# Kernel optimization log

Hardware: AMD Instinct MI355X
Metric: run time of the kernel (lower is better)

The kernel has to match this reference:

```python
import jax, jax.numpy as jnp
import numpy as np

CUT_DIST = 4.0            # cut_dist_bohr
FEATURES = 20
EPSILON = 1e-11
BOHR = 0.5291772105638411  # distance_mul (ase.units.Bohr)
POS_SCALE = 2.5


def setup_inputs() -> dict:
    key = jax.random.key(0)
    k1, k2 = jax.random.split(key)
    source = jax.random.normal(k1, (1, 4096, 3), dtype=jnp.float32) * POS_SCALE
    target = jax.random.normal(k2, (1, 2048, 3), dtype=jnp.float32) * POS_SCALE
    return {"source": source, "target": target}


def reference(source, target):
    # Pairwise diff between every source (probe) and target (atom): [B, N, M, 3]
    diff = target[:, None, :, :] - source[:, :, None, :]
    dist = jnp.sqrt(jnp.sum(diff * diff, axis=-1))            # [B, N, M]
    mask = dist < CUT_DIST                                    # [B, N, M] bool (self_send=True keeps d==0)
    direction = diff / (dist[..., None] + EPSILON)            # [B, N, M, 3]
    # sinc radial basis expansion on distances converted with distance_mul (Bohr)
    d = dist * BOHR + EPSILON                                 # [B, N, M]
    n = jnp.arange(1, FEATURES + 1, dtype=d.dtype)            # [F]
    d_exp = d[..., None]                                      # [B, N, M, 1]
    expansion = jnp.sin(n * jnp.pi * d_exp / CUT_DIST) / d_exp  # [B, N, M, F]
    return dist, direction, mask, expansion
```

## Files before the change

kernel.cpp:

```cpp
#include <hip/hip_runtime.h>
#include <math.h>

#define TILE 256
#define NFEAT 20

__global__ __launch_bounds__(256) void deepdft_expansion_kernel(
    const float* __restrict__ src,
    const float* __restrict__ tgt,
    float* __restrict__ out,
    unsigned int N, unsigned int M)
{
    const float CUT  = 4.0f;
    const float EPS  = 1e-11f;
    const float BOHR = 0.5291772105638411f;
    const float PI_F = 3.14159265358979323846f;

    const unsigned int total = N * M;

    float* __restrict__ dist_o = out;
    float* __restrict__ dir_o  = out + (size_t)total;
    float* __restrict__ mask_o = out + (size_t)4 * total;
    float* __restrict__ exp_o  = out + (size_t)5 * total;

    __shared__ float lds_dir[TILE * 3];
    __shared__ float lds_x[TILE];
    __shared__ float lds_invd[TILE];

    const unsigned int tid = threadIdx.x;
    const unsigned int tiles = (total + TILE - 1) / TILE;

    for (unsigned int tile = blockIdx.x; tile < tiles; tile += gridDim.x) {
        const unsigned int base = tile * TILE;
        const unsigned int idx  = base + tid;

        if (idx < total) {
            unsigned int n = idx / M;
            unsigned int m = idx - n * M;

            float sx = src[3u*n + 0], sy = src[3u*n + 1], sz = src[3u*n + 2];
            float tx = tgt[3u*m + 0], ty = tgt[3u*m + 1], tz = tgt[3u*m + 2];

            float dx = tx - sx, dy = ty - sy, dz = tz - sz;
            float d2   = fmaf(dx, dx, fmaf(dy, dy, dz * dz));
            float dist = sqrtf(d2);
            float inv  = 1.0f / (dist + EPS);

            dist_o[idx] = dist;
            mask_o[idx] = (dist < CUT) ? 1.0f : 0.0f;

            lds_dir[3u*tid + 0] = dx * inv;
            lds_dir[3u*tid + 1] = dy * inv;
            lds_dir[3u*tid + 2] = dz * inv;

            float d = fmaf(dist, BOHR, EPS);
            lds_invd[tid] = 1.0f / d;
            lds_x[tid]    = (PI_F / CUT) * d;
        }
        __syncthreads();

        {
            float* gdir = dir_o + (size_t)3 * base;
            #pragma unroll
            for (int k = 0; k < 3; ++k) {
                unsigned int e = tid + (unsigned)k * TILE;
                unsigned int p = (e * 10923u) >> 15;
                if (base + p < total) gdir[e] = lds_dir[e];
            }
        }

        {
            float4* gexp = reinterpret_cast<float4*>(exp_o + (size_t)NFEAT * base);
            #pragma unroll
            for (int k = 0; k < 5; ++k) {
                unsigned int j = tid + (unsigned)k * TILE;
                unsigned int p = (j * 6554u) >> 15;
                unsigned int g = j - 5u * p;
                if (base + p < total) {
                    float x    = lds_x[p];
                    float invd = lds_invd[p];
                    float n0   = (float)(4u * g + 1u);
                    float4 v;
                    v.x = __sinf( n0          * x) * invd;
                    v.y = __sinf((n0 + 1.0f)  * x) * invd;
                    v.z = __sinf((n0 + 2.0f)  * x) * invd;
                    v.w = __sinf((n0 + 3.0f)  * x) * invd;
                    gexp[j] = v;
                }
            }
        }
        __syncthreads();
    }
}

extern "C" void kernel_launch(void* const* d_in, const int* in_sizes, int n_in,
                              void* d_out, int out_size, void* d_ws, size_t ws_size,
                              hipStream_t stream) {
    const float* src = (const float*)d_in[0];
    const float* tgt = (const float*)d_in[1];
    float* out = (float*)d_out;

    unsigned int N = (unsigned int)(in_sizes[0] / 3);
    unsigned int M = (unsigned int)(in_sizes[1] / 3);
    unsigned int total = N * M;

    const unsigned int block = TILE;
    unsigned int tiles = (total + TILE - 1) / TILE;
    unsigned int blocks = tiles > 2048u ? 2048u : tiles;

    deepdft_expansion_kernel<<<blocks, block, 0, stream>>>(src, tgt, out, N, M);
}
```

Baseline: 159.7 us.

## Replace block LDS staging with per-wave tiles and ds_bpermute shuffles

Each wave now handles its own 64-element tile and redistributes per-pair values (direction components, x, 1/d) across lanes with ds_bpermute instead of staging them through shared memory. This removes the two block-wide __syncthreads per tile and the LDS arrays. The cost is extra bpermute instructions (three per direction store, two per expansion store) and per-lane select logic. Out-of-range lanes are clamped so the shuffles stay valid.

```diff
diff --git a/kernel.cpp b/kernel.cpp
--- a/kernel.cpp
+++ b/kernel.cpp
@@ -1,8 +1,12 @@
 #include <hip/hip_runtime.h>
 #include <math.h>
 
-#define TILE 256
 #define NFEAT 20
+
+__device__ __forceinline__ float bperm(unsigned int lane, float v) {
+    return __int_as_float(
+        __builtin_amdgcn_ds_bpermute((int)(lane << 2), __float_as_int(v)));
+}
 
 __global__ __launch_bounds__(256) void deepdft_expansion_kernel(
     const float* __restrict__ src,
@@ -22,73 +26,70 @@
     float* __restrict__ mask_o = out + (size_t)4 * total;
     float* __restrict__ exp_o  = out + (size_t)5 * total;
 
-    __shared__ float lds_dir[TILE * 3];
-    __shared__ float lds_x[TILE];
-    __shared__ float lds_invd[TILE];
+    const unsigned int lane = threadIdx.x & 63u;
+    const unsigned int wavesPerGrid = (gridDim.x * blockDim.x) >> 6;
+    const unsigned int wtiles = (total + 63u) >> 6;
 
-    const unsigned int tid = threadIdx.x;
-    const unsigned int tiles = (total + TILE - 1) / TILE;
+    for (unsigned int w = (blockIdx.x * blockDim.x + threadIdx.x) >> 6;
+         w < wtiles; w += wavesPerGrid) {
+        const unsigned int base = w << 6;
+        const unsigned int idx  = base + lane;
+        const unsigned int cidx = (idx < total) ? idx : (total - 1u);
 
-    for (unsigned int tile = blockIdx.x; tile < tiles; tile += gridDim.x) {
-        const unsigned int base = tile * TILE;
-        const unsigned int idx  = base + tid;
+        unsigned int n = cidx / M;
+        unsigned int m = cidx - n * M;
+
+        float sx = src[3u*n + 0], sy = src[3u*n + 1], sz = src[3u*n + 2];
+        float tx = tgt[3u*m + 0], ty = tgt[3u*m + 1], tz = tgt[3u*m + 2];
+
+        float dx = tx - sx, dy = ty - sy, dz = tz - sz;
+        float d2   = fmaf(dx, dx, fmaf(dy, dy, dz * dz));
+        float dist = sqrtf(d2);
+        float inv  = 1.0f / (dist + EPS);
 
         if (idx < total) {
-            unsigned int n = idx / M;
-            unsigned int m = idx - n * M;
-
-            float sx = src[3u*n + 0], sy = src[3u*n + 1], sz = src[3u*n + 2];
-            float tx = tgt[3u*m + 0], ty = tgt[3u*m + 1], tz = tgt[3u*m + 2];
-
-            float dx = tx - sx, dy = ty - sy, dz = tz - sz;
-            float d2   = fmaf(dx, dx, fmaf(dy, dy, dz * dz));
-            float dist = sqrtf(d2);
-            float inv  = 1.0f / (dist + EPS);
-
             dist_o[idx] = dist;
             mask_o[idx] = (dist < CUT) ? 1.0f : 0.0f;
+        }
 
-            lds_dir[3u*tid + 0] = dx * inv;
-            lds_dir[3u*tid + 1] = dy * inv;
-            lds_dir[3u*tid + 2] = dz * inv;
-
-            float d = fmaf(dist, BOHR, EPS);
-            lds_invd[tid] = 1.0f / d;
-            lds_x[tid]    = (PI_F / CUT) * d;
-        }
-        __syncthreads();
+        float ux = dx * inv, uy = dy * inv, uz = dz * inv;
+        float d    = fmaf(dist, BOHR, EPS);
+        float invd = 1.0f / d;
+        float x    = (PI_F / CUT) * d;
 
         {
             float* gdir = dir_o + (size_t)3 * base;
             #pragma unroll
             for (int k = 0; k < 3; ++k) {
-                unsigned int e = tid + (unsigned)k * TILE;
+                unsigned int e = lane + 64u * (unsigned)k;
                 unsigned int p = (e * 10923u) >> 15;
-                if (base + p < total) gdir[e] = lds_dir[e];
+                unsigned int c = e - 3u * p;
+                float vx = bperm(p, ux);
+                float vy = bperm(p, uy);
+                float vz = bperm(p, uz);
+                float val = (c == 0u) ? vx : ((c == 1u) ? vy : vz);
+                if (base + p < total) gdir[e] = val;
             }
         }
 
         {
-            float4* gexp = reinterpret_cast<float4*>(exp_o + (size_t)NFEAT * base);
+            float4* gexp = reinterpret_cast<float4*>(exp_o) + (size_t)5 * base;
             #pragma unroll
             for (int k = 0; k < 5; ++k) {
-                unsigned int j = tid + (unsigned)k * TILE;
+                unsigned int j = lane + 64u * (unsigned)k;
                 unsigned int p = (j * 6554u) >> 15;
                 unsigned int g = j - 5u * p;
-                if (base + p < total) {
-                    float x    = lds_x[p];
-                    float invd = lds_invd[p];
-                    float n0   = (float)(4u * g + 1u);
-                    float4 v;
-                    v.x = __sinf( n0          * x) * invd;
-                    v.y = __sinf((n0 + 1.0f)  * x) * invd;
-                    v.z = __sinf((n0 + 2.0f)  * x) * invd;
-                    v.w = __sinf((n0 + 3.0f)  * x) * invd;
-                    gexp[j] = v;
-                }
+                float xv = bperm(p, x);
+                float iv = bperm(p, invd);
+                float n0 = (float)(4u * g + 1u);
+                float4 v;
+                v.x = __sinf( n0         * xv) * iv;
+                v.y = __sinf((n0 + 1.0f) * xv) * iv;
+                v.z = __sinf((n0 + 2.0f) * xv) * iv;
+                v.w = __sinf((n0 + 3.0f) * xv) * iv;
+                if (base + p < total) gexp[j] = v;
             }
         }
-        __syncthreads();
     }
 }
 
@@ -103,9 +104,10 @@
     unsigned int M = (unsigned int)(in_sizes[1] / 3);
     unsigned int total = N * M;
 
-    const unsigned int block = TILE;
-    unsigned int tiles = (total + TILE - 1) / TILE;
-    unsigned int blocks = tiles > 2048u ? 2048u : tiles;
+    const unsigned int block = 256;
+    unsigned int wtiles = (total + 63u) >> 6;
+    unsigned int blocks = (wtiles + (block / 64) - 1) / (block / 64);
+    if (blocks > 2048u) blocks = 2048u;
 
     deepdft_expansion_kernel<<<blocks, block, 0, stream>>>(src, tgt, out, N, M);
 }
```

Measured after the change: 158.7 us. No clear change (-0.6%).
